# Performance work log

Hardware: AMD Instinct MI355X
Metric: run time of the kernel (lower is better)

The kernel has to match this reference:

```python
import jax, jax.numpy as jnp
import numpy as np
import math

B, S, D, H = 4, 1024, 512, 8
DK = D // H
NEG = -1e32


def setup_inputs() -> dict:
    key = jax.random.key(0)
    ks = jax.random.split(key, 16)
    f = lambda k, shape: jax.random.normal(k, shape, dtype=jnp.float32)
    w = 1.0 / math.sqrt(D)  # xavier-ish scale
    return {
        'query_mean': f(ks[0], (B, S, D)),
        'query_cov': f(ks[1], (B, S, D)),
        'key_mean': f(ks[2], (B, S, D)),
        'key_cov': f(ks[3], (B, S, D)),
        'values_mean': f(ks[4], (B, S, D)),
        'values_cov': f(ks[5], (B, S, D)),
        'Wk_mean': f(ks[6], (D, D)) * w, 'bk_mean': jnp.zeros((D,), jnp.float32),
        'Wk_cov': f(ks[7], (D, D)) * w, 'bk_cov': jnp.zeros((D,), jnp.float32),
        'Wv_mean': f(ks[8], (D, D)) * w, 'bv_mean': jnp.zeros((D,), jnp.float32),
        'Wv_cov': f(ks[9], (D, D)) * w, 'bv_cov': jnp.zeros((D,), jnp.float32),
        'Wo_mean': f(ks[10], (D, D)) * w, 'bo_mean': jnp.zeros((D,), jnp.float32),
        'Wo_cov': f(ks[11], (D, D)) * w, 'bo_cov': jnp.zeros((D,), jnp.float32),
        'gammas': f(ks[12], (H, 1, 1)) * 0.1,
        'mask': jnp.tril(jnp.ones((1, 1, S, S), dtype=jnp.int32)),
    }


def _forward(query_mean, query_cov, key_mean, key_cov, values_mean, values_cov,
             Wk_mean, bk_mean, Wk_cov, bk_cov, Wv_mean, bv_mean, Wv_cov, bv_cov,
             Wo_mean, bo_mean, Wo_cov, bo_cov, gammas, mask):
    def heads(x, W, b):  # [B,S,D] -> [B,H,S,DK]
        return (x @ W + b).reshape(B, S, H, DK).transpose(0, 2, 1, 3)

    # kq_same=True: queries and keys share the k linears
    qm = heads(query_mean, Wk_mean, bk_mean)
    qc = heads(query_cov, Wk_cov, bk_cov)
    km = heads(key_mean, Wk_mean, bk_mean)
    kc = heads(key_cov, Wk_cov, bk_cov)
    vm = heads(values_mean, Wv_mean, bv_mean)
    vc = heads(values_cov, Wv_cov, bv_cov)

    inv = 1.0 / math.sqrt(DK)
    sm = jnp.einsum('bhqd,bhkd->bhqk', qm, km) * inv  # [B,H,S,S]
    sc = jnp.einsum('bhqd,bhkd->bhqk', qc, kc) * inv

    maskf = mask.astype(jnp.float32)
    # position_effect[i,j] = |j - i|
    pos = jnp.abs(jnp.arange(S)[None, :] - jnp.arange(S)[:, None]).astype(jnp.float32)[None, None]

    def dist_scores(s):
        p = jax.nn.softmax(jnp.where(mask == 0, NEG, s), axis=-1) * maskf
        cum = jnp.cumsum(p, axis=-1)
        tot = jnp.sum(p, axis=-1, keepdims=True)
        return jnp.sqrt(jnp.clip((tot - cum) * pos, 0.0, None))

    dm = jax.lax.stop_gradient(dist_scores(sm))  # torch no_grad + detach
    dc = jax.lax.stop_gradient(dist_scores(sc))

    gv = -jax.nn.softplus(gammas)[None]  # [1,H,1,1]
    em = jnp.clip(jnp.exp(dm * gv), 1e-5, 1e5)
    ec = jnp.clip(jnp.exp(dc * gv), 1e-5, 1e5)

    am = jax.nn.softmax(jnp.where(mask == 0, NEG, sm * em), axis=-1)
    ac = jax.nn.softmax(jnp.where(mask == 0, NEG, sc * ec), axis=-1)

    om = jnp.einsum('bhqk,bhkd->bhqd', am, vm).transpose(0, 2, 1, 3).reshape(B, S, D)
    oc = jnp.einsum('bhqk,bhkd->bhqd', ac, vc).transpose(0, 2, 1, 3).reshape(B, S, D)
    return om @ Wo_mean + bo_mean, oc @ Wo_cov + bo_cov


def reference(query_mean, query_cov, key_mean, key_cov, values_mean, values_cov,
              Wk_mean, bk_mean, Wk_cov, bk_cov, Wv_mean, bv_mean, Wv_cov, bv_cov,
              Wo_mean, bo_mean, Wo_cov, bo_cov, gammas, mask):
    return _forward(query_mean, query_cov, key_mean, key_cov, values_mean, values_cov,
                    Wk_mean, bk_mean, Wk_cov, bk_cov, Wv_mean, bv_mean, Wv_cov, bv_cov,
                    Wo_mean, bo_mean, Wo_cov, bo_cov, gammas, mask)
```

## Files before the change

### kernel.cpp

```cpp
#include <hip/hip_runtime.h>
#include <hip/hip_bf16.h>
#include <math.h>

constexpr int B_  = 4;
constexpr int S_  = 1024;
constexpr int D_  = 512;
constexpr int H_  = 8;
constexpr int DK_ = 64;
constexpr int MROWS_ = B_ * S_;
constexpr size_t SZ_ = (size_t)B_ * H_ * S_ * DK_;
constexpr size_t WSZ_ = (size_t)D_ * D_;

typedef __attribute__((ext_vector_type(8))) short bf16x8;
typedef __attribute__((ext_vector_type(4))) float f32x4;

__device__ __forceinline__ float bf2f(unsigned short u) {
  union { unsigned int u; float f; } v; v.u = (unsigned int)u << 16; return v.f;
}
__device__ __forceinline__ unsigned short f2bf(float f) {
  union { float f; unsigned int u; } v; v.f = f;
  unsigned int r = v.u + 0x7FFFu + ((v.u >> 16) & 1u);
  return (unsigned short)(r >> 16);
}
__device__ __forceinline__ unsigned short f2bf_ru(float f) {
  union { float f; unsigned int u; } v; v.f = f;
  return (unsigned short)((v.u + 0x8000u) >> 16);
}

__device__ __forceinline__ float ex2(float x) {
#if __has_builtin(__builtin_amdgcn_exp2f)
  return __builtin_amdgcn_exp2f(x);
#else
  float r; asm("v_exp_f32 %0, %1" : "=v"(r) : "v"(x)); return r;
#endif
}
__device__ __forceinline__ float fsqrt_raw(float x) {
#if __has_builtin(__builtin_amdgcn_sqrtf)
  return __builtin_amdgcn_sqrtf(x);
#else
  float r; asm("v_sqrt_f32 %0, %1" : "=v"(r) : "v"(x)); return r;
#endif
}
__device__ __forceinline__ float frcp_raw(float x) {
#if __has_builtin(__builtin_amdgcn_rcpf)
  return __builtin_amdgcn_rcpf(x);
#else
  float r; asm("v_rcp_f32 %0, %1" : "=v"(r) : "v"(x)); return r;
#endif
}

template <int CTRL>
__device__ __forceinline__ float dpp_mov_f(float x) {
  return __builtin_bit_cast(float,
      __builtin_amdgcn_update_dpp(0, __builtin_bit_cast(int, x), CTRL, 0xF, 0xF, true));
}
__device__ __forceinline__ float scan16(float v) {
  v += dpp_mov_f<0x111>(v);
  v += dpp_mov_f<0x112>(v);
  v += dpp_mov_f<0x114>(v);
  v += dpp_mov_f<0x118>(v);
  return v;
}
__device__ __forceinline__ float red16(float v) {
  v += dpp_mov_f<0x128>(v);
  v += dpp_mov_f<0x124>(v);
  v += dpp_mov_f<0x122>(v);
  v += dpp_mov_f<0x121>(v);
  return v;
}
__device__ __forceinline__ float bcast15(float v) {
  return __builtin_bit_cast(float,
      __builtin_amdgcn_ds_swizzle(__builtin_bit_cast(int, v), 0x01F0));
}

__device__ __forceinline__ void gll16(const unsigned short* g, unsigned short* l) {
  __builtin_amdgcn_global_load_lds(
      (const __attribute__((address_space(1))) unsigned int*)g,
      (__attribute__((address_space(3))) unsigned int*)l, 16, 0, 0);
}

struct TpArgs { const float* W[4]; unsigned short* out[4]; };

__global__ __launch_bounds__(256) void wtrans(TpArgs a) {
  const int z = blockIdx.z;
  const float* __restrict__ W = a.W[z];
  unsigned short* __restrict__ out = a.out[z];
  __shared__ float T[64][65];
  const int tid = threadIdx.x;
  const int tx = blockIdx.x & 7, ty = blockIdx.x >> 3;
  const int k0 = ty * 64, n0 = tx * 64;
#pragma unroll
  for (int i = 0; i < 4; ++i) {
    const int idx = tid + i * 256;
    const int r = idx >> 4, c4 = (idx & 15) * 4;
    const float4 w = *(const float4*)&W[(size_t)(k0 + r) * D_ + n0 + c4];
    T[r][c4 + 0] = w.x; T[r][c4 + 1] = w.y; T[r][c4 + 2] = w.z; T[r][c4 + 3] = w.w;
  }
  __syncthreads();
#pragma unroll
  for (int i = 0; i < 4; ++i) {
    const int idx = tid + i * 256;
    const int n = idx >> 4, kc = (idx & 15) * 4;
    ushort4 pk;
    pk.x = f2bf(T[kc + 0][n]); pk.y = f2bf(T[kc + 1][n]);
    pk.z = f2bf(T[kc + 2][n]); pk.w = f2bf(T[kc + 3][n]);
    *(ushort4*)&out[(size_t)(n0 + n) * D_ + k0 + kc] = pk;
  }
}

struct ProjArgs {
  const float* A[6]; const unsigned short* Wt[6]; const float* bias[6];
  unsigned short* out[6]; int vmode[6];
};

__global__ __launch_bounds__(256) void proj_mfma(ProjArgs args) {
  const int z = blockIdx.z;
  const float* __restrict__ A = args.A[z];
  const unsigned short* __restrict__ Wt = args.Wt[z];
  const float* __restrict__ bias = args.bias[z];
  unsigned short* __restrict__ out = args.out[z];
  const int vmode = args.vmode[z];

  __shared__ unsigned short Abuf[128][40];
  __shared__ unsigned short Bbuf[128][32];
  const int tid = threadIdx.x, wv = tid >> 6, lane = tid & 63;
  const int quad = lane >> 4, l16 = lane & 15;
  const int wm = wv >> 1, wn = wv & 1;
  const int n0 = blockIdx.x * 128, m0 = blockIdx.y * 128;

  f32x4 acc[4][4];
#pragma unroll
  for (int i = 0; i < 4; ++i)
#pragma unroll
    for (int j = 0; j < 4; ++j) acc[i][j] = (f32x4){0.f, 0.f, 0.f, 0.f};

  for (int kt = 0; kt < 16; ++kt) {
    const int k0 = kt * 32;
    __syncthreads();
#pragma unroll
    for (int i = 0; i < 2; ++i) {
      const int idx = tid + i * 256;
      const int n = idx >> 2, c = idx & 3;
      gll16(&Wt[(size_t)(n0 + n) * D_ + k0 + c * 8], &Bbuf[n][c * 8]);
    }
#pragma unroll
    for (int i = 0; i < 4; ++i) {
      const int idx = tid + i * 256;
      const int m = idx >> 3, c = idx & 7;
      const float4 av = *(const float4*)&A[(size_t)(m0 + m) * D_ + k0 + c * 4];
      ushort4 p;
      p.x = f2bf(av.x); p.y = f2bf(av.y); p.z = f2bf(av.z); p.w = f2bf(av.w);
      *(ushort4*)&Abuf[m][c * 4] = p;
    }
    __syncthreads();

    bf16x8 af[4], bfr[4];
#pragma unroll
    for (int i = 0; i < 4; ++i) af[i] = *(const bf16x8*)&Abuf[wm * 64 + i * 16 + l16][quad * 8];
#pragma unroll
    for (int j = 0; j < 4; ++j) bfr[j] = *(const bf16x8*)&Bbuf[wn * 64 + j * 16 + l16][quad * 8];
#pragma unroll
    for (int i = 0; i < 4; ++i)
#pragma unroll
      for (int j = 0; j < 4; ++j)
        acc[i][j] = __builtin_amdgcn_mfma_f32_16x16x32_bf16(af[i], bfr[j], acc[i][j], 0, 0, 0);
  }

#pragma unroll
  for (int j = 0; j < 4; ++j) {
    const int col = n0 + wn * 64 + j * 16 + l16;
    const float bv = bias[col];
    const int h = col >> 6, dk = col & 63;
#pragma unroll
    for (int i = 0; i < 4; ++i) {
      const int mbase = m0 + wm * 64 + i * 16 + quad * 4;
      const int b = mbase >> 10;
      if (!vmode) {
#pragma unroll
        for (int r = 0; r < 4; ++r) {
          const int s = (mbase + r) & 1023;
          out[(((size_t)b * H_ + h) * S_ + s) * DK_ + dk] = f2bf(acc[i][j][r] + bv);
        }
      } else {
        const int s = mbase & 1023;
        ushort4 pk;
        pk.x = f2bf(acc[i][j][0] + bv); pk.y = f2bf(acc[i][j][1] + bv);
        pk.z = f2bf(acc[i][j][2] + bv); pk.w = f2bf(acc[i][j][3] + bv);
        *(ushort4*)&out[(((size_t)b * H_ + h) * DK_ + dk) * S_ + s] = pk;
      }
    }
  }
}

struct OutArgs {
  const unsigned short* A[2]; const unsigned short* Wt[2];
  const float* bias[2]; float* out[2];
};

__global__ __launch_bounds__(256) void out_mfma(OutArgs args) {
  const int z = blockIdx.z;
  const unsigned short* __restrict__ A = args.A[z];
  const unsigned short* __restrict__ Wt = args.Wt[z];
  const float* __restrict__ bias = args.bias[z];
  float* __restrict__ out = args.out[z];

  __shared__ unsigned short Abuf[128][32];
  __shared__ unsigned short Bbuf[128][32];
  const int tid = threadIdx.x, wv = tid >> 6, lane = tid & 63;
  const int quad = lane >> 4, l16 = lane & 15;
  const int wm = wv >> 1, wn = wv & 1;
  const int n0 = blockIdx.x * 128, m0 = blockIdx.y * 128;

  f32x4 acc[4][4];
#pragma unroll
  for (int i = 0; i < 4; ++i)
#pragma unroll
    for (int j = 0; j < 4; ++j) acc[i][j] = (f32x4){0.f, 0.f, 0.f, 0.f};

  for (int kt = 0; kt < 16; ++kt) {
    const int k0 = kt * 32;
    __syncthreads();
#pragma unroll
    for (int i = 0; i < 2; ++i) {
      const int idx = tid + i * 256;
      const int m = idx >> 2, c = idx & 3;
      gll16(&A[(size_t)(m0 + m) * D_ + k0 + c * 8], &Abuf[m][c * 8]);
    }
#pragma unroll
    for (int i = 0; i < 2; ++i) {
      const int idx = tid + i * 256;
      const int n = idx >> 2, c = idx & 3;
      gll16(&Wt[(size_t)(n0 + n) * D_ + k0 + c * 8], &Bbuf[n][c * 8]);
    }
    __syncthreads();

    bf16x8 af[4], bfr[4];
#pragma unroll
    for (int i = 0; i < 4; ++i) af[i] = *(const bf16x8*)&Abuf[wm * 64 + i * 16 + l16][quad * 8];
#pragma unroll
    for (int j = 0; j < 4; ++j) bfr[j] = *(const bf16x8*)&Bbuf[wn * 64 + j * 16 + l16][quad * 8];
#pragma unroll
    for (int i = 0; i < 4; ++i)
#pragma unroll
      for (int j = 0; j < 4; ++j)
        acc[i][j] = __builtin_amdgcn_mfma_f32_16x16x32_bf16(af[i], bfr[j], acc[i][j], 0, 0, 0);
  }

#pragma unroll
  for (int j = 0; j < 4; ++j) {
    const int col = n0 + wn * 64 + j * 16 + l16;
    const float bv = bias[col];
#pragma unroll
    for (int i = 0; i < 4; ++i) {
      const int mbase = m0 + wm * 64 + i * 16 + quad * 4;
#pragma unroll
      for (int r = 0; r < 4; ++r)
        out[(size_t)(mbase + r) * D_ + col] = acc[i][j][r] + bv;
    }
  }
}

__global__ __launch_bounds__(512) void attn_mfma(
    const unsigned short* __restrict__ qkv, const float* __restrict__ gammas,
    unsigned short* __restrict__ Obase)
{
  __shared__ unsigned short Ps[8][16][72];

  const int tid = threadIdx.x;
  const int w = tid >> 6, lane = tid & 63, quad = lane >> 4, l16 = lane & 15;
  const int bh = blockIdx.x;
  const int pair = blockIdx.y;
  const int ch = blockIdx.z;
  const int qt = (w < 4) ? (15 - pair) : pair;
  const int wq = w & 3;
  const int q0 = qt << 6;
  const int b = bh >> 3, h = bh & 7;

  constexpr float SC_ = 0.125f * 1.4426950408889634f;
  constexpr float LOG2E_ = 1.4426950408889634f;

  const unsigned short* Q  = qkv + (size_t)ch * 3 * SZ_ + (size_t)bh * S_ * DK_;
  const unsigned short* K  = qkv + (size_t)ch * 3 * SZ_ + SZ_ + (size_t)bh * S_ * DK_;
  const unsigned short* Vt = qkv + (size_t)ch * 3 * SZ_ + 2 * SZ_ + (size_t)bh * (size_t)DK_ * S_;
  unsigned short* O = Obase + (size_t)ch * SZ_;

  const float g = gammas[h];
  const float gv2 = -(fmaxf(g, 0.f) + log1pf(__expf(-fabsf(g)))) * LOG2E_;

  const unsigned short* Qrow = Q + (size_t)(q0 + wq * 16 + l16) * DK_;
  const bf16x8 qf0 = *(const bf16x8*)(Qrow + quad * 8);
  const bf16x8 qf1 = *(const bf16x8*)(Qrow + 32 + quad * 8);
  const int myrow = q0 + wq * 16 + quad * 4;

  float Tacc[4] = {0.f, 0.f, 0.f, 0.f};
  for (int kt = 0; kt <= qt; ++kt) {
    f32x4 sa[4];
#pragma unroll
    for (int cb = 0; cb < 4; ++cb) {
      const unsigned short* Kr = K + (size_t)(kt * 64 + cb * 16 + l16) * DK_;
      const bf16x8 kf0 = *(const bf16x8*)(Kr + quad * 8);
      const bf16x8 kf1 = *(const bf16x8*)(Kr + 32 + quad * 8);
      f32x4 a = {0.f, 0.f, 0.f, 0.f};
      a = __builtin_amdgcn_mfma_f32_16x16x32_bf16(qf0, kf0, a, 0, 0, 0);
      a = __builtin_amdgcn_mfma_f32_16x16x32_bf16(qf1, kf1, a, 0, 0, 0);
      sa[cb] = a;
    }
    if (kt == qt) {
#pragma unroll
      for (int cb = 0; cb < 4; ++cb)
#pragma unroll
        for (int r = 0; r < 4; ++r) {
          float e = ex2(sa[cb][r] * SC_);
          if ((kt * 64 + cb * 16 + l16) > (myrow + r)) e = 0.f;
          Tacc[r] += e;
        }
    } else {
#pragma unroll
      for (int cb = 0; cb < 4; ++cb)
#pragma unroll
        for (int r = 0; r < 4; ++r)
          Tacc[r] += ex2(sa[cb][r] * SC_);
    }
  }
  float invT[4];
#pragma unroll
  for (int r = 0; r < 4; ++r) invT[r] = frcp_raw(red16(Tacc[r]));

  float carry[4] = {0.f, 0.f, 0.f, 0.f};
  float l2a[4] = {0.f, 0.f, 0.f, 0.f};
  f32x4 oacc[4];
#pragma unroll
  for (int cb = 0; cb < 4; ++cb) oacc[cb] = (f32x4){0.f, 0.f, 0.f, 0.f};

  for (int kt = 0; kt <= qt; ++kt) {
    bf16x8 vf0[4], vf1[4];
#pragma unroll
    for (int cb = 0; cb < 4; ++cb) {
      const unsigned short* Vr = Vt + (size_t)(cb * 16 + l16) * S_ + kt * 64;
      vf0[cb] = *(const bf16x8*)(Vr + quad * 8);
      vf1[cb] = *(const bf16x8*)(Vr + 32 + quad * 8);
    }

    f32x4 sa[4];
#pragma unroll
    for (int cb = 0; cb < 4; ++cb) {
      const unsigned short* Kr = K + (size_t)(kt * 64 + cb * 16 + l16) * DK_;
      const bf16x8 kf0 = *(const bf16x8*)(Kr + quad * 8);
      const bf16x8 kf1 = *(const bf16x8*)(Kr + 32 + quad * 8);
      f32x4 a = {0.f, 0.f, 0.f, 0.f};
      a = __builtin_amdgcn_mfma_f32_16x16x32_bf16(qf0, kf0, a, 0, 0, 0);
      a = __builtin_amdgcn_mfma_f32_16x16x32_bf16(qf1, kf1, a, 0, 0, 0);
      sa[cb] = a;
    }
#pragma unroll
    for (int cb = 0; cb < 4; ++cb)
#pragma unroll
      for (int r = 0; r < 4; ++r) sa[cb][r] *= SC_;
    if (kt == qt) {
#pragma unroll
      for (int cb = 0; cb < 4; ++cb)
#pragma unroll
        for (int r = 0; r < 4; ++r)
          if ((kt * 64 + cb * 16 + l16) > (myrow + r)) sa[cb][r] = -1e30f;
    }

#pragma unroll
    for (int r = 0; r < 4; ++r) {
      float v0 = scan16(ex2(sa[0][r]));
      float v1 = scan16(ex2(sa[1][r]));
      float v2 = scan16(ex2(sa[2][r]));
      float v3 = scan16(ex2(sa[3][r]));
      const float tt0 = bcast15(v0), tt1 = bcast15(v1);
      const float tt2 = bcast15(v2), tt3 = bcast15(v3);
      const float base = carry[r];
      const float p01 = tt0 + tt1, p012 = p01 + tt2;
      const float cum0 = (base + v0) * invT[r];
      const float cum1 = (base + tt0 + v1) * invT[r];
      const float cum2 = (base + p01 + v2) * invT[r];
      const float cum3 = (base + p012 + v3) * invT[r];
      carry[r] = base + p012 + tt3;

      const float bpos = (float)(myrow + r) - (float)(kt * 64 + l16);
      float dd, st0, st1, st2, st3;
      dd = fsqrt_raw(fmaxf((1.f - cum0) * bpos, 0.f));
      st0 = sa[0][r] * fmaxf(ex2(dd * gv2), 1e-5f);
      dd = fsqrt_raw(fmaxf((1.f - cum1) * (bpos - 16.f), 0.f));
      st1 = sa[1][r] * fmaxf(ex2(dd * gv2), 1e-5f);
      dd = fsqrt_raw(fmaxf((1.f - cum2) * (bpos - 32.f), 0.f));
      st2 = sa[2][r] * fmaxf(ex2(dd * gv2), 1e-5f);
      dd = fsqrt_raw(fmaxf((1.f - cum3) * (bpos - 48.f), 0.f));
      st3 = sa[3][r] * fmaxf(ex2(dd * gv2), 1e-5f);

      const float w0 = ex2(st0), w1 = ex2(st1);
      const float w2 = ex2(st2), w3 = ex2(st3);
      l2a[r] += (w0 + w1) + (w2 + w3);
      const int prow = quad * 4 + r;
      Ps[w][prow][ 0 + l16] = f2bf_ru(w0);
      Ps[w][prow][16 + l16] = f2bf_ru(w1);
      Ps[w][prow][32 + l16] = f2bf_ru(w2);
      Ps[w][prow][48 + l16] = f2bf_ru(w3);
    }
    asm volatile("s_waitcnt lgkmcnt(0)" ::: "memory");

    const bf16x8 pf0 = *(const bf16x8*)&Ps[w][l16][quad * 8];
    const bf16x8 pf1 = *(const bf16x8*)&Ps[w][l16][32 + quad * 8];
#pragma unroll
    for (int cb = 0; cb < 4; ++cb) {
      oacc[cb] = __builtin_amdgcn_mfma_f32_16x16x32_bf16(pf0, vf0[cb], oacc[cb], 0, 0, 0);
      oacc[cb] = __builtin_amdgcn_mfma_f32_16x16x32_bf16(pf1, vf1[cb], oacc[cb], 0, 0, 0);
    }
  }

#pragma unroll
  for (int r = 0; r < 4; ++r) {
    const float inv = frcp_raw(red16(l2a[r]));
    const int srow = myrow + r;
    const size_t base = ((size_t)b * S_ + srow) * D_ + h * DK_;
    O[base +  0 + l16] = f2bf(oacc[0][r] * inv);
    O[base + 16 + l16] = f2bf(oacc[1][r] * inv);
    O[base + 32 + l16] = f2bf(oacc[2][r] * inv);
    O[base + 48 + l16] = f2bf(oacc[3][r] * inv);
  }
}

extern "C" void kernel_launch(void* const* d_in, const int* in_sizes, int n_in,
                              void* d_out, int out_size, void* d_ws, size_t ws_size,
                              hipStream_t stream) {
  const float* query_mean  = (const float*)d_in[0];
  const float* query_cov   = (const float*)d_in[1];
  const float* key_mean    = (const float*)d_in[2];
  const float* key_cov     = (const float*)d_in[3];
  const float* values_mean = (const float*)d_in[4];
  const float* values_cov  = (const float*)d_in[5];
  const float* Wk_mean = (const float*)d_in[6];
  const float* bk_mean = (const float*)d_in[7];
  const float* Wk_cov  = (const float*)d_in[8];
  const float* bk_cov  = (const float*)d_in[9];
  const float* Wv_mean = (const float*)d_in[10];
  const float* bv_mean = (const float*)d_in[11];
  const float* Wv_cov  = (const float*)d_in[12];
  const float* bv_cov  = (const float*)d_in[13];
  const float* Wo_mean = (const float*)d_in[14];
  const float* bo_mean = (const float*)d_in[15];
  const float* Wo_cov  = (const float*)d_in[16];
  const float* bo_cov  = (const float*)d_in[17];
  const float* gammas  = (const float*)d_in[18];

  unsigned short* qkv  = (unsigned short*)d_ws;
  unsigned short* obuf = qkv + 6 * SZ_;
  unsigned short* Wt4  = (unsigned short*)d_out;
  unsigned short* Wot  = qkv + 2 * SZ_;
  float* out = (float*)d_out;

  TpArgs t1;
  t1.W[0] = Wk_mean; t1.W[1] = Wv_mean; t1.W[2] = Wk_cov; t1.W[3] = Wv_cov;
  for (int i = 0; i < 4; ++i) t1.out[i] = Wt4 + (size_t)i * WSZ_;
  wtrans<<<dim3(64, 1, 4), 256, 0, stream>>>(t1);

  ProjArgs pa;
  const float* pA[6] = {query_mean, key_mean, values_mean, query_cov, key_cov, values_cov};
  const int   wIdx[6] = {0, 0, 1, 2, 2, 3};
  const float* pb[6] = {bk_mean, bk_mean, bv_mean, bk_cov, bk_cov, bv_cov};
  const int pv[6] = {0, 0, 1, 0, 0, 1};
  for (int i = 0; i < 6; ++i) {
    pa.A[i] = pA[i]; pa.Wt[i] = Wt4 + (size_t)wIdx[i] * WSZ_; pa.bias[i] = pb[i];
    pa.out[i] = qkv + (size_t)i * SZ_; pa.vmode[i] = pv[i];
  }
  proj_mfma<<<dim3(4, 32, 6), 256, 0, stream>>>(pa);

  attn_mfma<<<dim3(32, 8, 2), 512, 0, stream>>>(qkv, gammas, obuf);

  TpArgs t2;
  t2.W[0] = Wo_mean; t2.W[1] = Wo_cov; t2.W[2] = Wo_mean; t2.W[3] = Wo_cov;
  t2.out[0] = Wot; t2.out[1] = Wot + WSZ_; t2.out[2] = Wot; t2.out[3] = Wot + WSZ_;
  wtrans<<<dim3(64, 1, 2), 256, 0, stream>>>(t2);

  OutArgs oa;
  oa.A[0] = obuf;        oa.A[1] = obuf + SZ_;
  oa.Wt[0] = Wot;        oa.Wt[1] = Wot + WSZ_;
  oa.bias[0] = bo_mean;  oa.bias[1] = bo_cov;
  oa.out[0] = out;       oa.out[1] = out + (size_t)MROWS_ * D_;
  out_mfma<<<dim3(4, 32, 2), 256, 0, stream>>>(oa);
}
```

Measured before the change: 269.7 us.

## Split attention key range across two wave groups per query tile

Each block now handles a single query tile, and its two groups of four waves split the key tiles in half. They no longer work on paired complementary query tiles. The partial row sums are exchanged through shared memory so each group can compute a global normaliser and its cumulative-sum carry. Partial outputs and l2 sums are combined through shared memory, reusing the P buffer, before the store. The grid doubles to 16 tiles in y, which adds more blocks and finer work units at the cost of extra barriers and the combine step.

```diff
diff --git a/kernel.cpp b/kernel.cpp
--- a/kernel.cpp
+++ b/kernel.cpp
@@ -265,16 +265,25 @@
     unsigned short* __restrict__ Obase)
 {
   __shared__ unsigned short Ps[8][16][72];
+  __shared__ float Tpart[2][64];
+
+  float* const Cmb = (float*)&Ps[0][0][0];
+  float* const Cl2 = &Tpart[0][0];
 
   const int tid = threadIdx.x;
   const int w = tid >> 6, lane = tid & 63, quad = lane >> 4, l16 = lane & 15;
   const int bh = blockIdx.x;
-  const int pair = blockIdx.y;
+  const int qt = 15 - (int)blockIdx.y;
   const int ch = blockIdx.z;
-  const int qt = (w < 4) ? (15 - pair) : pair;
+  const int grp = w >> 2;
   const int wq = w & 3;
   const int q0 = qt << 6;
   const int b = bh >> 3, h = bh & 7;
+
+  const int nt = qt + 1;
+  const int mid = (nt + 1) >> 1;
+  const int t_lo = grp ? mid : 0;
+  const int t_hi = grp ? nt : mid;
 
   constexpr float SC_ = 0.125f * 1.4426950408889634f;
   constexpr float LOG2E_ = 1.4426950408889634f;
@@ -291,9 +300,10 @@
   const bf16x8 qf0 = *(const bf16x8*)(Qrow + quad * 8);
   const bf16x8 qf1 = *(const bf16x8*)(Qrow + 32 + quad * 8);
   const int myrow = q0 + wq * 16 + quad * 4;
+  const int rowb = wq * 16 + quad * 4;
 
   float Tacc[4] = {0.f, 0.f, 0.f, 0.f};
-  for (int kt = 0; kt <= qt; ++kt) {
+  for (int kt = t_lo; kt < t_hi; ++kt) {
     f32x4 sa[4];
 #pragma unroll
     for (int cb = 0; cb < 4; ++cb) {
@@ -322,17 +332,26 @@
           Tacc[r] += ex2(sa[cb][r] * SC_);
     }
   }
-  float invT[4];
-#pragma unroll
-  for (int r = 0; r < 4; ++r) invT[r] = frcp_raw(red16(Tacc[r]));
-
-  float carry[4] = {0.f, 0.f, 0.f, 0.f};
+#pragma unroll
+  for (int r = 0; r < 4; ++r)
+    Tpart[grp][rowb + r] = red16(Tacc[r]);
+  __syncthreads();
+
+  float invT[4], carry[4];
+#pragma unroll
+  for (int r = 0; r < 4; ++r) {
+    const float T0 = Tpart[0][rowb + r];
+    const float T1 = Tpart[1][rowb + r];
+    invT[r] = frcp_raw(T0 + T1);
+    carry[r] = grp ? T0 : 0.f;
+  }
+
   float l2a[4] = {0.f, 0.f, 0.f, 0.f};
   f32x4 oacc[4];
 #pragma unroll
   for (int cb = 0; cb < 4; ++cb) oacc[cb] = (f32x4){0.f, 0.f, 0.f, 0.f};
 
-  for (int kt = 0; kt <= qt; ++kt) {
+  for (int kt = t_lo; kt < t_hi; ++kt) {
     bf16x8 vf0[4], vf1[4];
 #pragma unroll
     for (int cb = 0; cb < 4; ++cb) {
@@ -411,15 +430,31 @@
     }
   }
 
-#pragma unroll
-  for (int r = 0; r < 4; ++r) {
-    const float inv = frcp_raw(red16(l2a[r]));
-    const int srow = myrow + r;
-    const size_t base = ((size_t)b * S_ + srow) * D_ + h * DK_;
-    O[base +  0 + l16] = f2bf(oacc[0][r] * inv);
-    O[base + 16 + l16] = f2bf(oacc[1][r] * inv);
-    O[base + 32 + l16] = f2bf(oacc[2][r] * inv);
-    O[base + 48 + l16] = f2bf(oacc[3][r] * inv);
+  __syncthreads();
+  if (grp == 1) {
+#pragma unroll
+    for (int r = 0; r < 4; ++r) {
+      const int row = rowb + r;
+      Cl2[row] = red16(l2a[r]);
+      Cmb[row * 65 +  0 + l16] = oacc[0][r];
+      Cmb[row * 65 + 16 + l16] = oacc[1][r];
+      Cmb[row * 65 + 32 + l16] = oacc[2][r];
+      Cmb[row * 65 + 48 + l16] = oacc[3][r];
+    }
+  }
+  __syncthreads();
+  if (grp == 0) {
+#pragma unroll
+    for (int r = 0; r < 4; ++r) {
+      const int row = rowb + r;
+      const float inv = frcp_raw(red16(l2a[r]) + Cl2[row]);
+      const int srow = q0 + row;
+      const size_t base = ((size_t)b * S_ + srow) * D_ + h * DK_;
+      O[base +  0 + l16] = f2bf((oacc[0][r] + Cmb[row * 65 +  0 + l16]) * inv);
+      O[base + 16 + l16] = f2bf((oacc[1][r] + Cmb[row * 65 + 16 + l16]) * inv);
+      O[base + 32 + l16] = f2bf((oacc[2][r] + Cmb[row * 65 + 32 + l16]) * inv);
+      O[base + 48 + l16] = f2bf((oacc[3][r] + Cmb[row * 65 + 48 + l16]) * inv);
+    }
   }
 }
 
@@ -468,7 +503,7 @@
   }
   proj_mfma<<<dim3(4, 32, 6), 256, 0, stream>>>(pa);
 
-  attn_mfma<<<dim3(32, 8, 2), 512, 0, stream>>>(qkv, gammas, obuf);
+  attn_mfma<<<dim3(32, 16, 2), 512, 0, stream>>>(qkv, gammas, obuf);
 
   TpArgs t2;
   t2.W[0] = Wo_mean; t2.W[1] = Wo_cov; t2.W[2] = Wo_mean; t2.W[3] = Wo_cov;
```

Measured after the change: 277.8 us. 3.0% more time.

## Pre-convert activations to bf16 and load them with async LDS copies

Applied to the files above, without the earlier changes.

Adds a separate kernel that converts the six fp32 input activations to bf16 in workspace. The projection GEMM can then load its A tiles through global_load_lds directly into LDS, the same way it already loads B, instead of converting in registers. The Wo weight transpose is folded into the first transpose launch, which removes one kernel launch. In exchange, the activations make an extra full round trip through global memory, and the A LDS tile loses its padding, which may cause bank conflicts.

```diff
diff --git a/kernel.cpp b/kernel.cpp
--- a/kernel.cpp
+++ b/kernel.cpp
@@ -79,7 +79,24 @@
       (__attribute__((address_space(3))) unsigned int*)l, 16, 0, 0);
 }
 
-struct TpArgs { const float* W[4]; unsigned short* out[4]; };
+struct CvtArgs { const float* src[6]; unsigned short* dst; };
+
+__global__ __launch_bounds__(256) void a2bf(CvtArgs a) {
+  const int z = blockIdx.z;
+  const float* __restrict__ src = a.src[z];
+  unsigned short* __restrict__ dst = a.dst + (size_t)z * MROWS_ * D_;
+  const int idx = blockIdx.x * 256 + threadIdx.x;
+#pragma unroll
+  for (int i = 0; i < 8; ++i) {
+    const size_t j = (size_t)idx + (size_t)i * 65536;
+    const float4 v = *(const float4*)&src[j * 4];
+    ushort4 p;
+    p.x = f2bf(v.x); p.y = f2bf(v.y); p.z = f2bf(v.z); p.w = f2bf(v.w);
+    *(ushort4*)&dst[j * 4] = p;
+  }
+}
+
+struct TpArgs { const float* W[6]; unsigned short* out[6]; };
 
 __global__ __launch_bounds__(256) void wtrans(TpArgs a) {
   const int z = blockIdx.z;
@@ -109,19 +126,19 @@
 }
 
 struct ProjArgs {
-  const float* A[6]; const unsigned short* Wt[6]; const float* bias[6];
+  const unsigned short* A[6]; const unsigned short* Wt[6]; const float* bias[6];
   unsigned short* out[6]; int vmode[6];
 };
 
 __global__ __launch_bounds__(256) void proj_mfma(ProjArgs args) {
   const int z = blockIdx.z;
-  const float* __restrict__ A = args.A[z];
+  const unsigned short* __restrict__ A = args.A[z];
   const unsigned short* __restrict__ Wt = args.Wt[z];
   const float* __restrict__ bias = args.bias[z];
   unsigned short* __restrict__ out = args.out[z];
   const int vmode = args.vmode[z];
 
-  __shared__ unsigned short Abuf[128][40];
+  __shared__ unsigned short Abuf[128][32];
   __shared__ unsigned short Bbuf[128][32];
   const int tid = threadIdx.x, wv = tid >> 6, lane = tid & 63;
   const int quad = lane >> 4, l16 = lane & 15;
@@ -140,17 +157,14 @@
 #pragma unroll
     for (int i = 0; i < 2; ++i) {
       const int idx = tid + i * 256;
+      const int m = idx >> 2, c = idx & 3;
+      gll16(&A[(size_t)(m0 + m) * D_ + k0 + c * 8], &Abuf[m][c * 8]);
+    }
+#pragma unroll
+    for (int i = 0; i < 2; ++i) {
+      const int idx = tid + i * 256;
       const int n = idx >> 2, c = idx & 3;
       gll16(&Wt[(size_t)(n0 + n) * D_ + k0 + c * 8], &Bbuf[n][c * 8]);
-    }
-#pragma unroll
-    for (int i = 0; i < 4; ++i) {
-      const int idx = tid + i * 256;
-      const int m = idx >> 3, c = idx & 7;
-      const float4 av = *(const float4*)&A[(size_t)(m0 + m) * D_ + k0 + c * 4];
-      ushort4 p;
-      p.x = f2bf(av.x); p.y = f2bf(av.y); p.z = f2bf(av.z); p.w = f2bf(av.w);
-      *(ushort4*)&Abuf[m][c * 4] = p;
     }
     __syncthreads();
 
@@ -448,32 +462,36 @@
 
   unsigned short* qkv  = (unsigned short*)d_ws;
   unsigned short* obuf = qkv + 6 * SZ_;
+  unsigned short* abf  = qkv + 8 * SZ_;
+  unsigned short* Wot  = qkv + 14 * SZ_;
   unsigned short* Wt4  = (unsigned short*)d_out;
-  unsigned short* Wot  = qkv + 2 * SZ_;
   float* out = (float*)d_out;
 
   TpArgs t1;
   t1.W[0] = Wk_mean; t1.W[1] = Wv_mean; t1.W[2] = Wk_cov; t1.W[3] = Wv_cov;
+  t1.W[4] = Wo_mean; t1.W[5] = Wo_cov;
   for (int i = 0; i < 4; ++i) t1.out[i] = Wt4 + (size_t)i * WSZ_;
-  wtrans<<<dim3(64, 1, 4), 256, 0, stream>>>(t1);
+  t1.out[4] = Wot; t1.out[5] = Wot + WSZ_;
+  wtrans<<<dim3(64, 1, 6), 256, 0, stream>>>(t1);
+
+  CvtArgs cv;
+  cv.src[0] = query_mean; cv.src[1] = key_mean; cv.src[2] = values_mean;
+  cv.src[3] = query_cov;  cv.src[4] = key_cov;  cv.src[5] = values_cov;
+  cv.dst = abf;
+  a2bf<<<dim3(256, 1, 6), 256, 0, stream>>>(cv);
 
   ProjArgs pa;
-  const float* pA[6] = {query_mean, key_mean, values_mean, query_cov, key_cov, values_cov};
   const int   wIdx[6] = {0, 0, 1, 2, 2, 3};
   const float* pb[6] = {bk_mean, bk_mean, bv_mean, bk_cov, bk_cov, bv_cov};
   const int pv[6] = {0, 0, 1, 0, 0, 1};
   for (int i = 0; i < 6; ++i) {
-    pa.A[i] = pA[i]; pa.Wt[i] = Wt4 + (size_t)wIdx[i] * WSZ_; pa.bias[i] = pb[i];
+    pa.A[i] = abf + (size_t)i * MROWS_ * D_;
+    pa.Wt[i] = Wt4 + (size_t)wIdx[i] * WSZ_; pa.bias[i] = pb[i];
     pa.out[i] = qkv + (size_t)i * SZ_; pa.vmode[i] = pv[i];
   }
   proj_mfma<<<dim3(4, 32, 6), 256, 0, stream>>>(pa);
 
   attn_mfma<<<dim3(32, 8, 2), 512, 0, stream>>>(qkv, gammas, obuf);
-
-  TpArgs t2;
-  t2.W[0] = Wo_mean; t2.W[1] = Wo_cov; t2.W[2] = Wo_mean; t2.W[3] = Wo_cov;
-  t2.out[0] = Wot; t2.out[1] = Wot + WSZ_; t2.out[2] = Wot; t2.out[3] = Wot + WSZ_;
-  wtrans<<<dim3(64, 1, 2), 256, 0, stream>>>(t2);
 
   OutArgs oa;
   oa.A[0] = obuf;        oa.A[1] = obuf + SZ_;
```

Result: no change. 265.0 us (median of 3 runs) (-1.7%).
